# Kernel optimization log

Measured on AMD Instinct MI355X. Metric: run time of the kernel, lower is better.

The kernel has to match this reference:

```python
import jax, jax.numpy as jnp
import numpy as np
from jax import lax

B, C, H, W = 4, 1024, 25, 25
CH = [1, 10, 10, 1]  # NeighConsensus channels
K = 3                # 4D kernel size (3,3,3,3)


def setup_inputs() -> dict:
    key = jax.random.key(0)
    ks = jax.random.split(key, 8)
    inp = {
        "feature_A": jax.random.normal(ks[0], (B, C, H, W), jnp.float32),
        "feature_B": jax.random.normal(ks[1], (B, C, H, W), jnp.float32),
    }
    for i in range(3):
        cin, cout = CH[i], CH[i + 1]
        scale = 1.0 / np.sqrt(cin * K ** 4)
        inp[f"W{i+1}"] = jax.random.normal(ks[2 + 2 * i], (cout, cin, K, K, K, K), jnp.float32) * scale
        inp[f"b{i+1}"] = jnp.zeros((cout,), jnp.float32)
    return inp


def feature_l2norm(x, axis=1):
    # torch: x / sqrt(sum(x^2, dim)+1e-6)
    return x / jnp.sqrt(jnp.sum(x * x, axis=axis, keepdims=True) + 1e-6)


# 4D convolution: lhs [B,C,f1,f2,f3,f4], rhs [Cout,Cin,k,k,k,k]
_DN = lax.ConvDimensionNumbers(lhs_spec=(0, 1, 2, 3, 4, 5),
                               rhs_spec=(0, 1, 2, 3, 4, 5),
                               out_spec=(0, 1, 2, 3, 4, 5))


def conv4d(x, w, b):
    p = K // 2
    y = lax.conv_general_dilated(x, w, (1, 1, 1, 1), [(p, p)] * 4, dimension_numbers=_DN)
    return y + b[None, :, None, None, None, None]


def nc_stack(x, Ws, bs):
    # Conv4d + ReLU stack (CreateCon4D)
    for w, b in zip(Ws, bs):
        x = jax.nn.relu(conv4d(x, w, b))
    return x


def neigh_consensus(x, Ws, bs):
    # symmetric_mode: conv(x) + permuted conv of the (AB)->(BA) swapped tensor
    perm = (0, 1, 4, 5, 2, 3)
    return nc_stack(x, Ws, bs) + jnp.transpose(nc_stack(jnp.transpose(x, perm), Ws, bs), perm)


def mutual_matching(corr):
    # corr: [B,1,f1,f2,f3,f4]
    eps = 1e-5
    max_B = jnp.max(corr, axis=(2, 3), keepdims=True)  # max over (f1,f2)
    max_A = jnp.max(corr, axis=(4, 5), keepdims=True)  # max over (f3,f4)
    return corr * (corr / (max_A + eps)) * (corr / (max_B + eps))


def correlation(fA, fB):
    # FeatureCorrelation with normalization=True
    corr = jnp.einsum('bchw,bcij->bhwij', fA, fB)[:, None]  # [B,1,hA,wA,hB,wB]
    corr = jax.nn.relu(corr)
    # featureL2Norm over the singleton channel dim == elementwise x/sqrt(x^2+eps)
    return corr / jnp.sqrt(corr * corr + 1e-6)


def reference(feature_A, feature_B, W1, b1, W2, b2, W3, b3):
    fA = feature_l2norm(feature_A)
    fB = feature_l2norm(feature_B)
    corr4d = correlation(fA, fB)
    corr4d = mutual_matching(corr4d)
    corr4d = neigh_consensus(corr4d, (W1, W2, W3), (b1, b2, b3))
    corr4d = mutual_matching(corr4d)
    return corr4d
```

## Files before the change

kernel.cpp:

```cpp
#include <hip/hip_runtime.h>
#include <math.h>

#define HWQ 625
#define NPOSQ 390625
#define NB 4
#define NCH 1024

typedef __attribute__((ext_vector_type(8))) short bf16x8;
typedef __attribute__((ext_vector_type(4))) float f32x4;

__device__ inline unsigned short f2bf(float x) {
    union { float f; unsigned int u; } c; c.f = x;
    unsigned int u = c.u;
    return (unsigned short)((u + 0x7fffu + ((u >> 16) & 1u)) >> 16);
}

__global__ void pack_misc_kernel(const float* __restrict__ W1, const float* __restrict__ b1,
                                 const float* __restrict__ b2,
                                 float* __restrict__ W1P, float* __restrict__ bL1,
                                 float* __restrict__ bL2)
{
    int t = blockIdx.x * blockDim.x + threadIdx.x;
    if (t < 1620) {
        int co = t % 20; int r = t / 20; int e = r / 9, t34 = r % 9;
        W1P[t] = (co < 10) ? W1[co * 81 + e * 9 + t34] : W1[(co - 10) * 81 + t34 * 9 + e];
    }
    if (t < 20) { bL1[t] = b1[t % 10]; bL2[t] = b2[t % 10]; }
}

__global__ void pack_mfma_w2_kernel(const float* __restrict__ W2,
                                    unsigned short* __restrict__ Ablob)
{
    int t = blockIdx.x * blockDim.x + threadIdx.x;
    if (t >= 54 * 64) return;
    int frag = t >> 6, lane = t & 63;
    int g = frag / 27; int r1 = frag % 27; int kstep = r1 / 9; int dd = r1 % 9;
    int d3 = dd / 3, d4 = dd % 3;
    int co = lane & 15;
    unsigned short v[8];
#pragma unroll
    for (int j = 0; j < 8; ++j) {
        int k = kstep * 32 + ((lane >> 4) << 3) + j;
        float w = 0.0f;
        if (co < 10 && k < 90) {
            int ci = k / 9, e = k % 9, d1 = e / 3, d2 = e % 3;
            int tap = (g == 0) ? (d1 * 27 + d2 * 9 + d3 * 3 + d4)
                               : (d3 * 27 + d4 * 9 + d1 * 3 + d2);
            w = W2[(co * 10 + ci) * 81 + tap];
        }
        v[j] = f2bf(w);
    }
    uint4 val;
    val.x = (unsigned)v[0] | ((unsigned)v[1] << 16);
    val.y = (unsigned)v[2] | ((unsigned)v[3] << 16);
    val.z = (unsigned)v[4] | ((unsigned)v[5] << 16);
    val.w = (unsigned)v[6] | ((unsigned)v[7] << 16);
    *(uint4*)(Ablob + (size_t)frag * 512 + lane * 8) = val;
}

__global__ void pack_mfma_w3_kernel(const float* __restrict__ W3,
                                    unsigned short* __restrict__ Ablob3)
{
    int t = blockIdx.x * blockDim.x + threadIdx.x;
    if (t >= 54 * 64) return;
    int frag = t >> 6, lane = t & 63;
    int kstep = frag / 9, dd = frag % 9;
    int d3 = dd / 3, d4 = dd % 3;
    int row = lane & 15;
    unsigned short v[8];
#pragma unroll
    for (int j = 0; j < 8; ++j) {
        int k = kstep * 32 + ((lane >> 4) << 3) + j;
        float w = 0.0f;
        if (k < 180) {
            int g = k / 90, rem = k - g * 90;
            int ci = rem / 9, e = rem % 9;
            if (row == g) {
                int d1 = e / 3, d2 = e % 3;
                int tap = (g == 0) ? (d1 * 27 + d2 * 9 + d3 * 3 + d4)
                                   : (d3 * 27 + d4 * 9 + d1 * 3 + d2);
                w = W3[ci * 81 + tap];
            }
        }
        v[j] = f2bf(w);
    }
    uint4 val;
    val.x = (unsigned)v[0] | ((unsigned)v[1] << 16);
    val.y = (unsigned)v[2] | ((unsigned)v[3] << 16);
    val.z = (unsigned)v[4] | ((unsigned)v[5] << 16);
    val.w = (unsigned)v[6] | ((unsigned)v[7] << 16);
    *(uint4*)(Ablob3 + (size_t)frag * 512 + lane * 8) = val;
}

__global__ void invnorm_kernel(const float* __restrict__ fA, const float* __restrict__ fB,
                               float* __restrict__ invA, float* __restrict__ invB)
{
    int idx = blockIdx.x * blockDim.x + threadIdx.x;
    if (idx >= NB * HWQ) return;
    const float* f = blockIdx.y ? fB : fA;
    float* o = blockIdx.y ? invB : invA;
    int b = idx / HWQ, m = idx - b * HWQ;
    const float* p = f + (size_t)b * NCH * HWQ + m;
    float s = 0.f;
    for (int c = 0; c < NCH; c += 4) {
        float x0 = p[(c + 0) * HWQ], x1 = p[(c + 1) * HWQ];
        float x2 = p[(c + 2) * HWQ], x3 = p[(c + 3) * HWQ];
        s += x0 * x0 + x1 * x1 + x2 * x2 + x3 * x3;
    }
    o[idx] = 1.0f / sqrtf(s + 1e-6f);
}

__global__ __launch_bounds__(256) void corr_gemm_kernel(
    const float* __restrict__ fA, const float* __restrict__ fB,
    const float* __restrict__ invA, const float* __restrict__ invB,
    float* __restrict__ corr)
{
    __shared__ float As[16][64];
    __shared__ float Bs[16][64];
    const int b = blockIdx.z;
    const int m0 = blockIdx.y * 64, n0 = blockIdx.x * 64;
    const int tid = threadIdx.x;
    const int tx = tid & 15, ty = tid >> 4;
    float acc[4][4] = {};
    const float* Ab = fA + (size_t)b * NCH * HWQ;
    const float* Bb = fB + (size_t)b * NCH * HWQ;
    for (int k0 = 0; k0 < NCH; k0 += 16) {
        for (int i = tid; i < 1024; i += 256) {
            int k = i >> 6, mm = i & 63;
            int gm = m0 + mm, gn = n0 + mm;
            As[k][mm] = (gm < HWQ) ? Ab[(k0 + k) * HWQ + gm] : 0.0f;
            Bs[k][mm] = (gn < HWQ) ? Bb[(k0 + k) * HWQ + gn] : 0.0f;
        }
        __syncthreads();
#pragma unroll
        for (int k = 0; k < 16; ++k) {
            float4 a4 = *(const float4*)&As[k][ty * 4];
            float4 b4 = *(const float4*)&Bs[k][tx * 4];
            float av[4] = {a4.x, a4.y, a4.z, a4.w};
            float bv[4] = {b4.x, b4.y, b4.z, b4.w};
#pragma unroll
            for (int i = 0; i < 4; ++i)
#pragma unroll
                for (int j = 0; j < 4; ++j)
                    acc[i][j] = fmaf(av[i], bv[j], acc[i][j]);
        }
        __syncthreads();
    }
#pragma unroll
    for (int i = 0; i < 4; ++i) {
        int m = m0 + ty * 4 + i;
        if (m >= HWQ) continue;
        float ia = invA[b * HWQ + m];
#pragma unroll
        for (int j = 0; j < 4; ++j) {
            int n = n0 + tx * 4 + j;
            if (n >= HWQ) continue;
            float v = acc[i][j] * ia * invB[b * HWQ + n];
            v = fmaxf(v, 0.0f);
            v = v / sqrtf(v * v + 1e-6f);
            corr[((size_t)b * HWQ + m) * HWQ + n] = v;
        }
    }
}

__global__ void rowmax_kernel(const float* __restrict__ s, float* __restrict__ rmax)
{
    int row = blockIdx.x * 4 + (threadIdx.x >> 6);
    int lane = threadIdx.x & 63;
    if (row >= NB * HWQ) return;
    const float* p = s + (size_t)row * HWQ;
    float v = -1e30f;
    for (int n = lane; n < HWQ; n += 64) v = fmaxf(v, p[n]);
    for (int off = 32; off; off >>= 1) v = fmaxf(v, __shfl_xor(v, off));
    if (lane == 0) rmax[row] = v;
// ... 31 lines not shown
    const float* in = corr + (size_t)blockIdx.z * NPOSQ;
    unsigned short* out = x1 + (size_t)blockIdx.z * 20 * NPOSQ;
    const int f1 = f12 / 25, f2 = f12 - f1 * 25;
    const int tid = threadIdx.x;

    for (int i = tid; i < 9 * 784; i += 192) sp[i] = 0.0f;
    for (int i = tid; i < 1620; i += 192) wl[i] = W1P[i];

    const int tt = (tid < 169) ? tid : 0;
    const int ty = tt / 13, tx = tt - ty * 13;
    const int r0 = ty * 2, c0 = tx * 2;

    float acc[20][4];
#pragma unroll
    for (int co = 0; co < 20; ++co) {
        float bv = bL1[co];
        acc[co][0] = bv; acc[co][1] = bv; acc[co][2] = bv; acc[co][3] = bv;
    }

    __syncthreads();
    for (int i = tid; i < 5625; i += 192) {
        int e = i / 625, q = i - e * 625;
        int d1 = e / 3, d2 = e - d1 * 3;
        int f1n = f1 + d1 - 1, f2n = f2 + d2 - 1;
        float v = 0.0f;
        if (((unsigned)f1n < 25u) & ((unsigned)f2n < 25u))
            v = in[(f1n * 25 + f2n) * HWQ + q];
        int rr = q / 25, cc = q - rr * 25;
        sp[e * 784 + (rr + 1) * 28 + (cc + 1)] = v;
    }
    __syncthreads();

#pragma unroll 1
    for (int e = 0; e < 9; ++e) {
        float win[16];
        const int base = e * 784 + r0 * 28 + c0;
#pragma unroll
        for (int a = 0; a < 4; ++a)
#pragma unroll
            for (int bb = 0; bb < 4; ++bb)
                win[a * 4 + bb] = sp[base + a * 28 + bb];
#pragma unroll
        for (int t34 = 0; t34 < 9; ++t34) {
            int d3 = t34 / 3, d4 = t34 - d3 * 3;
            float x0 = win[d3 * 4 + d4], x1v = win[d3 * 4 + d4 + 1];
            float x2v = win[(d3 + 1) * 4 + d4], x3v = win[(d3 + 1) * 4 + d4 + 1];
            const float* wp = wl + (e * 9 + t34) * 20;
#pragma unroll
            for (int c4 = 0; c4 < 5; ++c4) {
                float4 w4 = *(const float4*)(wp + c4 * 4);
                float wv[4] = {w4.x, w4.y, w4.z, w4.w};
#pragma unroll
                for (int q4 = 0; q4 < 4; ++q4) {
                    int co = c4 * 4 + q4;
                    acc[co][0] = fmaf(x0, wv[q4], acc[co][0]);
                    acc[co][1] = fmaf(x1v, wv[q4], acc[co][1]);
                    acc[co][2] = fmaf(x2v, wv[q4], acc[co][2]);
                    acc[co][3] = fmaf(x3v, wv[q4], acc[co][3]);
                }
            }
        }
    }

    if (tid < 169) {
        unsigned short* ob = out + (size_t)f12 * 20 * 625;
#pragma unroll
        for (int co = 0; co < 20; ++co) {
            unsigned short* op = ob + co * 625;
#pragma unroll
            for (int i = 0; i < 2; ++i)
#pragma unroll
                for (int j = 0; j < 2; ++j) {
                    int f3 = r0 + i, f4 = c0 + j;
                    if (f3 < 25 && f4 < 25)
                        op[f3 * 25 + f4] = f2bf(fmaxf(acc[co][i * 2 + j], 0.0f));
                }
        }
    }
}

#define L2S 36
#define L2ROWS 736

#define STAGE_PRE()                                                         \
    int dstw_[10];                                                          \
    _Pragma("unroll")                                                       \
    for (int pass = 0; pass < 10; ++pass) {                                 \
        int idx = pass * 64 + lane;                                         \
        int rr = idx / 25, cc = idx - rr * 25;                              \
        dstw_[pass] = ((rr + 1) * 27 + cc + 1) * (L2S * 2) + wave * 8;      \
    }                                                                       \
    unsigned bpo_[7];                                                       \
    _Pragma("unroll")                                                       \
    for (int j = 0; j < 7; ++j) {                                           \
        int t = wave + j * 8;                                               \
        int f3 = t >> 1, h = t & 1;                                         \
        bpo_[j] = (unsigned)(((f3 * 27 + h * 16 + lo16) * L2S + kqg) * 2);  \
    }

#define STAGE_KSTEP(INPTR, CHOFF, CIE_MAX)                                  \
    _Pragma("unroll")                                                       \
    for (int i = 0; i < 4; ++i) {                                           \
        int cie = ksbase + wave * 4 + i;                                    \
        int ci = cie / 9, e = cie - ci * 9;                                 \
        int f1n = f1 + e / 3 - 1, f2n = f2 + (e - (e / 3) * 3) - 1;         \
        bool valid = (cie < (CIE_MAX)) & ((unsigned)f1n < 25u) & ((unsigned)f2n < 25u); \
        int pidx = valid ? ((f1n * 25 + f2n) * 20 + (CHOFF) + ci) : 0;      \
        const unsigned short* gp = (INPTR) + (size_t)pidx * 625;            \
        _Pragma("unroll")                                                   \
        for (int pass = 0; pass < 10; ++pass) {                             \
            if (pass < 9 || lane < 49) {                                    \
                unsigned short v = valid ? gp[pass * 64 + lane] : (unsigned short)0; \
                *(unsigned short*)((char*)sp + (dstw_[pass] + i * 2)) = v;  \
            }                                                               \
        }                                                                   \
    }

#define MFMA_KSTEP(ABASE)                                                   \
    {                                                                       \
        bf16x8 afA = *(const bf16x8*)(ABASE);                               \
        _Pragma("unroll")                                                   \
        for (int dd = 0; dd < 9; ++dd) {                                    \
            bf16x8 afN = (dd < 8) ? *(const bf16x8*)((ABASE) + (dd + 1) * 512) : afA; \
            const int d3 = dd / 3, d4 = dd - d3 * 3;                        \
            const int imm = (d3 * 27 + d4) * (L2S * 2);                     \
            _Pragma("unroll")                                               \
            for (int j = 0; j < 7; ++j) {                                   \
                if (j < 6 || wave < 2) {                                    \
                    const char* rp = (const char*)sp + (bpo_[j] + imm);     \
                    uint2 p0 = *(const uint2*)rp;                           \
                    uint2 p1 = *(const uint2*)(rp + 8);                     \
                    union { unsigned u[4]; bf16x8 v; } cv;                  \
                    cv.u[0] = p0.x; cv.u[1] = p0.y; cv.u[2] = p1.x; cv.u[3] = p1.y; \
                    acc[j] = __builtin_amdgcn_mfma_f32_16x16x32_bf16(afA, cv.v, acc[j], 0, 0, 0); \
                }                                                           \
            }                                                               \
            afA = afN;                                                      \
        }                                                                   \
    }

__global__ __launch_bounds__(512) void conv4d_mfma_l2(
    const unsigned short* __restrict__ x1, const unsigned short* __restrict__ Ablob,
    const float* __restrict__ bL2, unsigned short* __restrict__ x2)
{
    __shared__ alignas(16) unsigned short sp[L2ROWS * L2S];
    const int f12 = blockIdx.x, g = blockIdx.y;
    const unsigned short* in = x1 + (size_t)blockIdx.z * 20 * NPOSQ;
    unsigned short* out = x2 + (size_t)blockIdx.z * 20 * NPOSQ;
    const int f1 = f12 / 25, f2 = f12 - f1 * 25;
    const int tid = threadIdx.x, wave = tid >> 6, lane = tid & 63;
    const int lo16 = lane & 15, kqg = (lane >> 4) << 3;

    for (int i = tid; i < L2ROWS * L2S / 2; i += 512) ((unsigned*)sp)[i] = 0u;

    f32x4 acc[7];
#pragma unroll
    for (int j = 0; j < 7; ++j) acc[j] = (f32x4){0.f, 0.f, 0.f, 0.f};
    const unsigned short* Ag = Ablob + (size_t)g * 27 * 512;

    STAGE_PRE();

#pragma unroll 1
    for (int kstep = 0; kstep < 3; ++kstep) {
        const int ksbase = kstep * 32;
        __syncthreads();
        STAGE_KSTEP(in, g * 10, 90);
        __syncthreads();
        const unsigned short* Abase = Ag + (size_t)(kstep * 9) * 512 + lane * 8;
        MFMA_KSTEP(Abase);
    }

    unsigned short* ob = out + (size_t)f12 * 20 * 625 + g * 10 * 625;
    int t = wave;
    for (int j = 0; j < 7; ++j, t += 8) {
        if (t < 50) {
            int f3 = t >> 1, h = t & 1;
            int f4 = h * 16 + lo16;
            if (f4 < 25) {
#pragma unroll
                for (int r = 0; r < 4; ++r) {
                    int co = (lane >> 4) * 4 + r;
                    if (co < 10) {
                        float v = acc[j][r] + bL2[g * 10 + co];
                        ob[co * 625 + f3 * 25 + f4] = f2bf(fmaxf(v, 0.0f));
                    }
                }
            }
        }
    }
}

__global__ __launch_bounds__(512) void conv4d_mfma_l3(
    const unsigned short* __restrict__ x2, const unsigned short* __restrict__ Ablob3,
    const float* __restrict__ b3p, float* __restrict__ sbuf)
{
    __shared__ alignas(16) unsigned short sp[L2ROWS * L2S];
    const int f12 = blockIdx.x;
    const unsigned short* in = x2 + (size_t)blockIdx.z * 20 * NPOSQ;
    float* out = sbuf + (size_t)blockIdx.z * NPOSQ;
    const int f1 = f12 / 25, f2 = f12 - f1 * 25;
    const int tid = threadIdx.x, wave = tid >> 6, lane = tid & 63;
    const int lo16 = lane & 15, kqg = (lane >> 4) << 3;

    for (int i = tid; i < L2ROWS * L2S / 2; i += 512) ((unsigned*)sp)[i] = 0u;

    f32x4 acc[7];
#pragma unroll
    for (int j = 0; j < 7; ++j) acc[j] = (f32x4){0.f, 0.f, 0.f, 0.f};

    STAGE_PRE();

#pragma unroll 1
    for (int kstep = 0; kstep < 6; ++kstep) {
        const int ksbase = kstep * 32;
        __syncthreads();
        STAGE_KSTEP(in, 0, 180);
        __syncthreads();
        const unsigned short* Abase = Ablob3 + (size_t)(kstep * 9) * 512 + lane * 8;
        MFMA_KSTEP(Abase);
    }

    const float b3v = b3p[0];
    if ((lane >> 4) == 0) {
        int t = wave;
        for (int j = 0; j < 7; ++j, t += 8) {
            if (t < 50) {
                int f3 = t >> 1, h = t & 1;
                int f4 = h * 16 + lo16;
                if (f4 < 25) {
                    float s0 = fmaxf(acc[j][0] + b3v, 0.0f);
                    float s1 = fmaxf(acc[j][1] + b3v, 0.0f);
                    out[f12 * 625 + f3 * 25 + f4] = s0 + s1;
                }
            }
        }
    }
}

extern "C" void kernel_launch(void* const* d_in, const int* in_sizes, int n_in,
                              void* d_out, int out_size, void* d_ws, size_t ws_size,
                              hipStream_t stream)
{
    const float* fA = (const float*)d_in[0];
    const float* fB = (const float*)d_in[1];
    const float* W1 = (const float*)d_in[2];
    const float* b1 = (const float*)d_in[3];
    const float* W2 = (const float*)d_in[4];
    const float* b2 = (const float*)d_in[5];
    const float* W3 = (const float*)d_in[6];
    const float* b3 = (const float*)d_in[7];
    float* out = (float*)d_out;
    float* ws = (float*)d_ws;

    float* invA = ws + 0;
    float* invB = ws + 2500;
    float* rmax = ws + 5000;
    float* cmax = ws + 7500;
    float* W1P  = ws + 10000;
    float* bL1  = ws + 11620;
    float* bL2  = ws + 11640;
    unsigned short* Ablob2 = (unsigned short*)(ws + 12000);
    unsigned short* Ablob3 = (unsigned short*)(ws + 25824);
    float* corr = ws + 40000;
    float* sbuf = ws + 1602500;
    unsigned short* x1b = (unsigned short*)(ws + 3165000);

    const size_t REQ = (size_t)34415000 * 4;
    const bool fused = ws_size >= REQ;
    unsigned short* x2b = fused ? (unsigned short*)(ws + 18790000)
                                : (unsigned short*)(ws + 7080000);

    hipLaunchKernelGGL(pack_misc_kernel, dim3(7), dim3(256), 0, stream, W1, b1, b2, W1P, bL1, bL2);
    hipLaunchKernelGGL(pack_mfma_w2_kernel, dim3(14), dim3(256), 0, stream, W2, Ablob2);
    hipLaunchKernelGGL(pack_mfma_w3_kernel, dim3(14), dim3(256), 0, stream, W3, Ablob3);
    hipLaunchKernelGGL(invnorm_kernel, dim3(10, 2), dim3(256), 0, stream, fA, fB, invA, invB);
    hipLaunchKernelGGL(corr_gemm_kernel, dim3(10, 10, 4), dim3(256), 0, stream,
                       fA, fB, invA, invB, corr);
    hipLaunchKernelGGL(rowmax_kernel, dim3(625), dim3(256), 0, stream, corr, rmax);
    hipLaunchKernelGGL(colmax_kernel, dim3(4, 5), dim3(128), 0, stream, corr, cmax);
    hipLaunchKernelGGL(mm_apply_kernel, dim3(6104), dim3(256), 0, stream, corr, rmax, cmax, corr);

    if (fused) {
        hipLaunchKernelGGL(conv4d_l1, dim3(625, 1, NB), dim3(192), 0, stream, corr, W1P, bL1, x1b);
        hipLaunchKernelGGL(conv4d_mfma_l2, dim3(625, 2, NB), dim3(512), 0, stream,
                           x1b, Ablob2, bL2, x2b);
        hipLaunchKernelGGL(conv4d_mfma_l3, dim3(625, 1, NB), dim3(512), 0, stream,
                           x2b, Ablob3, b3, sbuf);
    } else {
        for (int b = 0; b < NB; ++b) {
            hipLaunchKernelGGL(conv4d_l1, dim3(625, 1, 1), dim3(192), 0, stream,
                               corr + (size_t)b * NPOSQ, W1P, bL1, x1b);
            hipLaunchKernelGGL(conv4d_mfma_l2, dim3(625, 2, 1), dim3(512), 0, stream,
                               x1b, Ablob2, bL2, x2b);
            hipLaunchKernelGGL(conv4d_mfma_l3, dim3(625, 1, 1), dim3(512), 0, stream,
                               x2b, Ablob3, b3, sbuf + (size_t)b * NPOSQ);
        }
    }

    hipLaunchKernelGGL(rowmax_kernel, dim3(625), dim3(256), 0, stream, sbuf, rmax);
    hipLaunchKernelGGL(colmax_kernel, dim3(4, 5), dim3(128), 0, stream, sbuf, cmax);
    hipLaunchKernelGGL(mm_apply_kernel, dim3(6104), dim3(256), 0, stream, sbuf, rmax, cmax, out);
}
```

Measured before the change: 1.265 ms.

## Prefetch L2 conv inputs into registers and replace L3 MFMA with VALU conv

```diff
diff --git a/kernel.cpp b/kernel.cpp
--- a/kernel.cpp
+++ b/kernel.cpp
@@ -14,16 +14,22 @@
     unsigned int u = c.u;
     return (unsigned short)((u + 0x7fffu + ((u >> 16) & 1u)) >> 16);
 }
+__device__ inline float bfl(unsigned u) { union { unsigned v; float f; } c; c.v = u << 16; return c.f; }
+__device__ inline float bfh(unsigned u) { union { unsigned v; float f; } c; c.v = u & 0xffff0000u; return c.f; }
 
 __global__ void pack_misc_kernel(const float* __restrict__ W1, const float* __restrict__ b1,
-                                 const float* __restrict__ b2,
-                                 float* __restrict__ W1P, float* __restrict__ bL1,
-                                 float* __restrict__ bL2)
+                                 const float* __restrict__ b2, const float* __restrict__ W3,
+                                 float* __restrict__ W1P, float* __restrict__ W3V,
+                                 float* __restrict__ bL1, float* __restrict__ bL2)
 {
     int t = blockIdx.x * blockDim.x + threadIdx.x;
     if (t < 1620) {
         int co = t % 20; int r = t / 20; int e = r / 9, t34 = r % 9;
         W1P[t] = (co < 10) ? W1[co * 81 + e * 9 + t34] : W1[(co - 10) * 81 + t34 * 9 + e];
+    }
+    if (t < 1620) {
+        int g = t / 810; int rem = t - g * 810; int ci = rem / 81; int tap = rem - ci * 81;
+        W3V[t] = W3[ci * 81 + (g == 0 ? tap : (tap % 9) * 9 + tap / 9)];
     }
     if (t < 20) { bL1[t] = b1[t % 10]; bL2[t] = b2[t % 10]; }
 }
@@ -56,40 +62,6 @@
     val.z = (unsigned)v[4] | ((unsigned)v[5] << 16);
     val.w = (unsigned)v[6] | ((unsigned)v[7] << 16);
     *(uint4*)(Ablob + (size_t)frag * 512 + lane * 8) = val;
-}
-
-__global__ void pack_mfma_w3_kernel(const float* __restrict__ W3,
-                                    unsigned short* __restrict__ Ablob3)
-{
-    int t = blockIdx.x * blockDim.x + threadIdx.x;
-    if (t >= 54 * 64) return;
-    int frag = t >> 6, lane = t & 63;
-    int kstep = frag / 9, dd = frag % 9;
-    int d3 = dd / 3, d4 = dd % 3;
-    int row = lane & 15;
-    unsigned short v[8];
-#pragma unroll
-    for (int j = 0; j < 8; ++j) {
-        int k = kstep * 32 + ((lane >> 4) << 3) + j;
-        float w = 0.0f;
-        if (k < 180) {
-            int g = k / 90, rem = k - g * 90;
-            int ci = rem / 9, e = rem % 9;
-            if (row == g) {
-                int d1 = e / 3, d2 = e % 3;
-                int tap = (g == 0) ? (d1 * 27 + d2 * 9 + d3 * 3 + d4)
-                                   : (d3 * 27 + d4 * 9 + d1 * 3 + d2);
-                w = W3[ci * 81 + tap];
-            }
-        }
-        v[j] = f2bf(w);
-    }
-    uint4 val;
-    val.x = (unsigned)v[0] | ((unsigned)v[1] << 16);
-    val.y = (unsigned)v[2] | ((unsigned)v[3] << 16);
-    val.z = (unsigned)v[4] | ((unsigned)v[5] << 16);
-    val.w = (unsigned)v[6] | ((unsigned)v[7] << 16);
-    *(uint4*)(Ablob3 + (size_t)frag * 512 + lane * 8) = val;
 }
 
 __global__ void invnorm_kernel(const float* __restrict__ fA, const float* __restrict__ fB,
@@ -287,60 +259,30 @@
 #define L2S 36
 #define L2ROWS 736
 
-#define STAGE_PRE()                                                         \
-    int dstw_[10];                                                          \
+#define L2_CALC(KS)                                                         \
+    {                                                                       \
+        int ksb = (KS) * 32;                                                \
+        _Pragma("unroll")                                                   \
+        for (int i2 = 0; i2 < 4; ++i2) {                                    \
+            int cie = ksb + wave * 4 + i2;                                  \
+            int ci = cie / 9, e = cie - ci * 9;                             \
+            int f1n = f1 + e / 3 - 1, f2n = f2 + (e - (e / 3) * 3) - 1;     \
+            bool valid = (cie < 90) & ((unsigned)f1n < 25u) & ((unsigned)f2n < 25u); \
+            int pidx = valid ? ((f1n * 25 + f2n) * 20 + g * 10 + ci) : 0;   \
+            gpp[i2] = in + (size_t)pidx * 625;                              \
+            vld[i2] = valid;                                                \
+        }                                                                   \
+    }
+
+#define L2_LOAD()                                                           \
     _Pragma("unroll")                                                       \
     for (int pass = 0; pass < 10; ++pass) {                                 \
-        int idx = pass * 64 + lane;                                         \
-        int rr = idx / 25, cc = idx - rr * 25;                              \
-        dstw_[pass] = ((rr + 1) * 27 + cc + 1) * (L2S * 2) + wave * 8;      \
-    }                                                                       \
-    unsigned bpo_[7];                                                       \
-    _Pragma("unroll")                                                       \
-    for (int j = 0; j < 7; ++j) {                                           \
-        int t = wave + j * 8;                                               \
-        int f3 = t >> 1, h = t & 1;                                         \
-        bpo_[j] = (unsigned)(((f3 * 27 + h * 16 + lo16) * L2S + kqg) * 2);  \
-    }
-
-#define STAGE_KSTEP(INPTR, CHOFF, CIE_MAX)                                  \
-    _Pragma("unroll")                                                       \
-    for (int i = 0; i < 4; ++i) {                                           \
-        int cie = ksbase + wave * 4 + i;                                    \
-        int ci = cie / 9, e = cie - ci * 9;                                 \
-        int f1n = f1 + e / 3 - 1, f2n = f2 + (e - (e / 3) * 3) - 1;         \
-        bool valid = (cie < (CIE_MAX)) & ((unsigned)f1n < 25u) & ((unsigned)f2n < 25u); \
-        int pidx = valid ? ((f1n * 25 + f2n) * 20 + (CHOFF) + ci) : 0;      \
-        const unsigned short* gp = (INPTR) + (size_t)pidx * 625;            \
-        _Pragma("unroll")                                                   \
-        for (int pass = 0; pass < 10; ++pass) {                             \
-            if (pass < 9 || lane < 49) {                                    \
-                unsigned short v = valid ? gp[pass * 64 + lane] : (unsigned short)0; \
-                *(unsigned short*)((char*)sp + (dstw_[pass] + i * 2)) = v;  \
-            }                                                               \
-        }                                                                   \
-    }
-
-#define MFMA_KSTEP(ABASE)                                                   \
-    {                                                                       \
-        bf16x8 afA = *(const bf16x8*)(ABASE);                               \
-        _Pragma("unroll")                                                   \
-        for (int dd = 0; dd < 9; ++dd) {                                    \
-            bf16x8 afN = (dd < 8) ? *(const bf16x8*)((ABASE) + (dd + 1) * 512) : afA; \
-            const int d3 = dd / 3, d4 = dd - d3 * 3;                        \
-            const int imm = (d3 * 27 + d4) * (L2S * 2);                     \
-            _Pragma("unroll")                                               \
-            for (int j = 0; j < 7; ++j) {                                   \
-                if (j < 6 || wave < 2) {                                    \
-                    const char* rp = (const char*)sp + (bpo_[j] + imm);     \
-                    uint2 p0 = *(const uint2*)rp;                           \
-                    uint2 p1 = *(const uint2*)(rp + 8);                     \
-                    union { unsigned u[4]; bf16x8 v; } cv;                  \
-                    cv.u[0] = p0.x; cv.u[1] = p0.y; cv.u[2] = p1.x; cv.u[3] = p1.y; \
-                    acc[j] = __builtin_amdgcn_mfma_f32_16x16x32_bf16(afA, cv.v, acc[j], 0, 0, 0); \
-                }                                                           \
-            }                                                               \
-            afA = afN;                                                      \
+        if (pass < 9 || lane < 49) {                                        \
+            int q = pass * 64 + lane;                                       \
+            vreg[pass][0] = vld[0] ? gpp[0][q] : (unsigned short)0;         \
+            vreg[pass][1] = vld[1] ? gpp[1][q] : (unsigned short)0;         \
+            vreg[pass][2] = vld[2] ? gpp[2][q] : (unsigned short)0;         \
+            vreg[pass][3] = vld[3] ? gpp[3][q] : (unsigned short)0;         \
         }                                                                   \
     }
 
@@ -363,16 +305,66 @@
     for (int j = 0; j < 7; ++j) acc[j] = (f32x4){0.f, 0.f, 0.f, 0.f};
     const unsigned short* Ag = Ablob + (size_t)g * 27 * 512;
 
-    STAGE_PRE();
+    int dstw_[10];
+#pragma unroll
+    for (int pass = 0; pass < 10; ++pass) {
+        int idx = pass * 64 + lane;
+        int rr = idx / 25, cc = idx - rr * 25;
+        dstw_[pass] = ((rr + 1) * 27 + cc + 1) * (L2S * 2) + wave * 8;
+    }
+    unsigned bpo_[7];
+#pragma unroll
+    for (int j = 0; j < 7; ++j) {
+        int t = wave + j * 8;
+        int f3 = t >> 1, h = t & 1;
+        bpo_[j] = (unsigned)(((f3 * 27 + h * 16 + lo16) * L2S + kqg) * 2);
+    }
+
+    const unsigned short* gpp[4];
+    bool vld[4];
+    unsigned short vreg[10][4];
+
+    L2_CALC(0);
+    L2_LOAD();
 
 #pragma unroll 1
     for (int kstep = 0; kstep < 3; ++kstep) {
-        const int ksbase = kstep * 32;
         __syncthreads();
-        STAGE_KSTEP(in, g * 10, 90);
+#pragma unroll
+        for (int pass = 0; pass < 10; ++pass) {
+            if (pass < 9 || lane < 49) {
+                uint2 w;
+                w.x = (unsigned)vreg[pass][0] | ((unsigned)vreg[pass][1] << 16);
+                w.y = (unsigned)vreg[pass][2] | ((unsigned)vreg[pass][3] << 16);
+                *(uint2*)((char*)sp + dstw_[pass]) = w;
+            }
+        }
         __syncthreads();
         const unsigned short* Abase = Ag + (size_t)(kstep * 9) * 512 + lane * 8;
-        MFMA_KSTEP(Abase);
+        bf16x8 af[9];
+#pragma unroll
+        for (int dd = 0; dd < 9; ++dd)
+            af[dd] = *(const bf16x8*)(Abase + dd * 512);
+        if (kstep < 2) {
+            L2_CALC(kstep + 1);
+            L2_LOAD();
+        }
+#pragma unroll
+        for (int dd = 0; dd < 9; ++dd) {
+            const int d3 = dd / 3, d4 = dd - d3 * 3;
+            const int imm = (d3 * 27 + d4) * (L2S * 2);
+#pragma unroll
+            for (int j = 0; j < 7; ++j) {
+                if (j < 6 || wave < 2) {
+                    const char* rp = (const char*)sp + (bpo_[j] + imm);
+                    uint2 p0 = *(const uint2*)rp;
+                    uint2 p1 = *(const uint2*)(rp + 8);
+                    union { unsigned u[4]; bf16x8 v; } cv;
+                    cv.u[0] = p0.x; cv.u[1] = p0.y; cv.u[2] = p1.x; cv.u[3] = p1.y;
+                    acc[j] = __builtin_amdgcn_mfma_f32_16x16x32_bf16(af[dd], cv.v, acc[j], 0, 0, 0);
+                }
+            }
+        }
     }
 
     unsigned short* ob = out + (size_t)f12 * 20 * 625 + g * 10 * 625;
@@ -395,50 +387,89 @@
     }
 }
 
-__global__ __launch_bounds__(512) void conv4d_mfma_l3(
-    const unsigned short* __restrict__ x2, const unsigned short* __restrict__ Ablob3,
+__global__ __launch_bounds__(192) void conv4d_l3_valu(
+    const unsigned short* __restrict__ x2, const float* __restrict__ W3V,
     const float* __restrict__ b3p, float* __restrict__ sbuf)
 {
-    __shared__ alignas(16) unsigned short sp[L2ROWS * L2S];
+    __shared__ unsigned short spb[2 * 9 * 784];
+    __shared__ float wl[1620];
     const int f12 = blockIdx.x;
     const unsigned short* in = x2 + (size_t)blockIdx.z * 20 * NPOSQ;
     float* out = sbuf + (size_t)blockIdx.z * NPOSQ;
     const int f1 = f12 / 25, f2 = f12 - f1 * 25;
-    const int tid = threadIdx.x, wave = tid >> 6, lane = tid & 63;
-    const int lo16 = lane & 15, kqg = (lane >> 4) << 3;
-
-    for (int i = tid; i < L2ROWS * L2S / 2; i += 512) ((unsigned*)sp)[i] = 0u;
-
-    f32x4 acc[7];
-#pragma unroll
-    for (int j = 0; j < 7; ++j) acc[j] = (f32x4){0.f, 0.f, 0.f, 0.f};
-
-    STAGE_PRE();
+    const int tid = threadIdx.x;
+
+    for (int i = tid; i < 2 * 9 * 784; i += 192) spb[i] = 0;
+    for (int i = tid; i < 1620; i += 192) wl[i] = W3V[i];
+
+    const int tt = (tid < 169) ? tid : 0;
+    const int ty = tt / 13, tx = tt - ty * 13;
+    const int r0 = ty * 2, c0 = tx * 2;
+
+    float acc0[4] = {0.f, 0.f, 0.f, 0.f}, acc1[4] = {0.f, 0.f, 0.f, 0.f};
 
 #pragma unroll 1
-    for (int kstep = 0; kstep < 6; ++kstep) {
-        const int ksbase = kstep * 32;
+    for (int ci = 0; ci < 10; ++ci) {
         __syncthreads();
-        STAGE_KSTEP(in, 0, 180);
+        for (int i = tid; i < 11250; i += 192) {
+            int plane = i / 625, q = i - plane * 625;
+            int gg = plane / 9, e = plane - gg * 9;
+            int d1 = e / 3, d2 = e - d1 * 3;
+            int f1n = f1 + d1 - 1, f2n = f2 + d2 - 1;
+            unsigned short v = 0;
+            if (((unsigned)f1n < 25u) & ((unsigned)f2n < 25u))
+                v = in[((size_t)(f1n * 25 + f2n) * 20 + gg * 10 + ci) * 625 + q];
+            int rr = q / 25, cc = q - rr * 25;
+            spb[plane * 784 + (rr + 1) * 28 + cc + 1] = v;
+        }
         __syncthreads();
-        const unsigned short* Abase = Ablob3 + (size_t)(kstep * 9) * 512 + lane * 8;
-        MFMA_KSTEP(Abase);
+        const float* w0p = wl + ci * 81;
+        const float* w1p = wl + (10 + ci) * 81;
+#pragma unroll 1
+        for (int e = 0; e < 9; ++e) {
+            float wa[16], wb[16];
+            const int base = e * 784 + r0 * 28 + c0;
+            const unsigned* pA = (const unsigned*)(spb + base);
+            const unsigned* pB = (const unsigned*)(spb + 9 * 784 + base);
+#pragma unroll
+            for (int a = 0; a < 4; ++a) {
+                unsigned uA0 = pA[a * 14], uA1 = pA[a * 14 + 1];
+                unsigned uB0 = pB[a * 14], uB1 = pB[a * 14 + 1];
+                wa[a * 4 + 0] = bfl(uA0); wa[a * 4 + 1] = bfh(uA0);
+                wa[a * 4 + 2] = bfl(uA1); wa[a * 4 + 3] = bfh(uA1);
+                wb[a * 4 + 0] = bfl(uB0); wb[a * 4 + 1] = bfh(uB0);
+                wb[a * 4 + 2] = bfl(uB1); wb[a * 4 + 3] = bfh(uB1);
+            }
+#pragma unroll
+            for (int t34 = 0; t34 < 9; ++t34) {
+                int d3 = t34 / 3, d4 = t34 - d3 * 3;
+                float g0w = w0p[e * 9 + t34];
+                float g1w = w1p[e * 9 + t34];
+                acc0[0] = fmaf(wa[d3 * 4 + d4],           g0w, acc0[0]);
+                acc0[1] = fmaf(wa[d3 * 4 + d4 + 1],       g0w, acc0[1]);
+                acc0[2] = fmaf(wa[(d3 + 1) * 4 + d4],     g0w, acc0[2]);
+                acc0[3] = fmaf(wa[(d3 + 1) * 4 + d4 + 1], g0w, acc0[3]);
+                acc1[0] = fmaf(wb[d3 * 4 + d4],           g1w, acc1[0]);
+                acc1[1] = fmaf(wb[d3 * 4 + d4 + 1],       g1w, acc1[1]);
+                acc1[2] = fmaf(wb[(d3 + 1) * 4 + d4],     g1w, acc1[2]);
+                acc1[3] = fmaf(wb[(d3 + 1) * 4 + d4 + 1], g1w, acc1[3]);
+            }
+        }
     }
 
     const float b3v = b3p[0];
-    if ((lane >> 4) == 0) {
-        int t = wave;
-        for (int j = 0; j < 7; ++j, t += 8) {
-            if (t < 50) {
-                int f3 = t >> 1, h = t & 1;
-                int f4 = h * 16 + lo16;
-                if (f4 < 25) {
-                    float s0 = fmaxf(acc[j][0] + b3v, 0.0f);
-                    float s1 = fmaxf(acc[j][1] + b3v, 0.0f);
-                    out[f12 * 625 + f3 * 25 + f4] = s0 + s1;
+    if (tid < 169) {
+#pragma unroll
+        for (int i = 0; i < 2; ++i)
+#pragma unroll
+            for (int j = 0; j < 2; ++j) {
+                int f3 = r0 + i, f4 = c0 + j;
+                if (f3 < 25 && f4 < 25) {
+                    int qi = i * 2 + j;
+                    out[f12 * 625 + f3 * 25 + f4] =
+                        fmaxf(acc0[qi] + b3v, 0.0f) + fmaxf(acc1[qi] + b3v, 0.0f);
                 }
             }
-        }
     }
 }
 
@@ -465,7 +496,7 @@
     float* bL1  = ws + 11620;
     float* bL2  = ws + 11640;
     unsigned short* Ablob2 = (unsigned short*)(ws + 12000);
-    unsigned short* Ablob3 = (unsigned short*)(ws + 25824);
+    float* W3V  = ws + 25824;
     float* corr = ws + 40000;
     float* sbuf = ws + 1602500;
     unsigned short* x1b = (unsigned short*)(ws + 3165000);
@@ -475,9 +506,9 @@
     unsigned short* x2b = fused ? (unsigned short*)(ws + 18790000)
                                 : (unsigned short*)(ws + 7080000);
 
-    hipLaunchKernelGGL(pack_misc_kernel, dim3(7), dim3(256), 0, stream, W1, b1, b2, W1P, bL1, bL2);
+    hipLaunchKernelGGL(pack_misc_kernel, dim3(7), dim3(256), 0, stream,
+                       W1, b1, b2, W3, W1P, W3V, bL1, bL2);
     hipLaunchKernelGGL(pack_mfma_w2_kernel, dim3(14), dim3(256), 0, stream, W2, Ablob2);
-    hipLaunchKernelGGL(pack_mfma_w3_kernel, dim3(14), dim3(256), 0, stream, W3, Ablob3);
     hipLaunchKernelGGL(invnorm_kernel, dim3(10, 2), dim3(256), 0, stream, fA, fB, invA, invB);
     hipLaunchKernelGGL(corr_gemm_kernel, dim3(10, 10, 4), dim3(256), 0, stream,
                        fA, fB, invA, invB, corr);
@@ -489,16 +520,16 @@
         hipLaunchKernelGGL(conv4d_l1, dim3(625, 1, NB), dim3(192), 0, stream, corr, W1P, bL1, x1b);
         hipLaunchKernelGGL(conv4d_mfma_l2, dim3(625, 2, NB), dim3(512), 0, stream,
                            x1b, Ablob2, bL2, x2b);
-        hipLaunchKernelGGL(conv4d_mfma_l3, dim3(625, 1, NB), dim3(512), 0, stream,
-                           x2b, Ablob3, b3, sbuf);
+        hipLaunchKernelGGL(conv4d_l3_valu, dim3(625, 1, NB), dim3(192), 0, stream,
+                           x2b, W3V, b3, sbuf);
     } else {
         for (int b = 0; b < NB; ++b) {
             hipLaunchKernelGGL(conv4d_l1, dim3(625, 1, 1), dim3(192), 0, stream,
                                corr + (size_t)b * NPOSQ, W1P, bL1, x1b);
             hipLaunchKernelGGL(conv4d_mfma_l2, dim3(625, 2, 1), dim3(512), 0, stream,
                                x1b, Ablob2, bL2, x2b);
-            hipLaunchKernelGGL(conv4d_mfma_l3, dim3(625, 1, 1), dim3(512), 0, stream,
-                               x2b, Ablob3, b3, sbuf + (size_t)b * NPOSQ);
+            hipLaunchKernelGGL(conv4d_l3_valu, dim3(625, 1, 1), dim3(192), 0, stream,
+                               x2b, W3V, b3, sbuf + (size_t)b * NPOSQ);
         }
     }
 
```

After: 1.586 ms. 1.25x slower.

## Prefetch next k-step global loads into registers while running MFMAs

Applied to the files above, without the earlier changes.

```diff
diff --git a/kernel.cpp b/kernel.cpp
--- a/kernel.cpp
+++ b/kernel.cpp
@@ -287,7 +287,7 @@
 #define L2S 36
 #define L2ROWS 736
 
-#define STAGE_PRE()                                                         \
+#define MF_PRE()                                                            \
     int dstw_[10];                                                          \
     _Pragma("unroll")                                                       \
     for (int pass = 0; pass < 10; ++pass) {                                 \
@@ -301,46 +301,64 @@
         int t = wave + j * 8;                                               \
         int f3 = t >> 1, h = t & 1;                                         \
         bpo_[j] = (unsigned)(((f3 * 27 + h * 16 + lo16) * L2S + kqg) * 2);  \
-    }
-
-#define STAGE_KSTEP(INPTR, CHOFF, CIE_MAX)                                  \
+    }                                                                       \
+    const unsigned short* gpp[4];                                           \
+    bool vld[4];                                                            \
+    unsigned short vreg[10][4];
+
+#define MF_CALC(KS, CHOFF, CIE_MAX)                                         \
+    {                                                                       \
+        int ksb = (KS) * 32;                                                \
+        _Pragma("unroll")                                                   \
+        for (int i2 = 0; i2 < 4; ++i2) {                                    \
+            int cie = ksb + wave * 4 + i2;                                  \
+            int e = cie % 9;                                                \
+            int f1n = f1 + e / 3 - 1, f2n = f2 + (e - (e / 3) * 3) - 1;     \
+            bool valid = (cie < (CIE_MAX)) & ((unsigned)f1n < 25u) & ((unsigned)f2n < 25u); \
+            int pidx = valid ? ((f1n * 25 + f2n) * 20 + (CHOFF) + cie / 9) : 0; \
+            gpp[i2] = in + (size_t)pidx * 625;                              \
+            vld[i2] = valid;                                                \
+        }                                                                   \
+    }
+
+#define MF_LOAD()                                                           \
     _Pragma("unroll")                                                       \
-    for (int i = 0; i < 4; ++i) {                                           \
-        int cie = ksbase + wave * 4 + i;                                    \
-        int ci = cie / 9, e = cie - ci * 9;                                 \
-        int f1n = f1 + e / 3 - 1, f2n = f2 + (e - (e / 3) * 3) - 1;         \
-        bool valid = (cie < (CIE_MAX)) & ((unsigned)f1n < 25u) & ((unsigned)f2n < 25u); \
-        int pidx = valid ? ((f1n * 25 + f2n) * 20 + (CHOFF) + ci) : 0;      \
-        const unsigned short* gp = (INPTR) + (size_t)pidx * 625;            \
+    for (int pass = 0; pass < 10; ++pass) {                                 \
+        if (pass < 9 || lane < 49) {                                        \
+            int q = pass * 64 + lane;                                       \
+            vreg[pass][0] = vld[0] ? gpp[0][q] : (unsigned short)0;         \
+            vreg[pass][1] = vld[1] ? gpp[1][q] : (unsigned short)0;         \
+            vreg[pass][2] = vld[2] ? gpp[2][q] : (unsigned short)0;         \
+            vreg[pass][3] = vld[3] ? gpp[3][q] : (unsigned short)0;         \
+        }                                                                   \
+    }
+
+#define MF_WRITE()                                                          \
+    _Pragma("unroll")                                                       \
+    for (int pass = 0; pass < 10; ++pass) {                                 \
+        if (pass < 9 || lane < 49) {                                        \
+            uint2 w;                                                        \
+            w.x = (unsigned)vreg[pass][0] | ((unsigned)vreg[pass][1] << 16);\
+            w.y = (unsigned)vreg[pass][2] | ((unsigned)vreg[pass][3] << 16);\
+            *(uint2*)((char*)sp + dstw_[pass]) = w;                         \
+        }                                                                   \
+    }
+
+#define MF_MFMA(AF)                                                         \
+    _Pragma("unroll")                                                       \
+    for (int dd = 0; dd < 9; ++dd) {                                        \
+        const int d3 = dd / 3, d4 = dd - d3 * 3;                            \
+        const int imm = (d3 * 27 + d4) * (L2S * 2);                         \
         _Pragma("unroll")                                                   \
-        for (int pass = 0; pass < 10; ++pass) {                             \
-            if (pass < 9 || lane < 49) {                                    \
-                unsigned short v = valid ? gp[pass * 64 + lane] : (unsigned short)0; \
-                *(unsigned short*)((char*)sp + (dstw_[pass] + i * 2)) = v;  \
+        for (int j = 0; j < 7; ++j) {                                       \
+            if (j < 6 || wave < 2) {                                        \
+                const char* rp = (const char*)sp + (bpo_[j] + imm);         \
+                uint2 p0 = *(const uint2*)rp;                               \
+                uint2 p1 = *(const uint2*)(rp + 8);                         \
+                union { unsigned u[4]; bf16x8 v; } cv;                      \
+                cv.u[0] = p0.x; cv.u[1] = p0.y; cv.u[2] = p1.x; cv.u[3] = p1.y; \
+                acc[j] = __builtin_amdgcn_mfma_f32_16x16x32_bf16((AF)[dd], cv.v, acc[j], 0, 0, 0); \
             }                                                               \
-        }                                                                   \
-    }
-
-#define MFMA_KSTEP(ABASE)                                                   \
-    {                                                                       \
-        bf16x8 afA = *(const bf16x8*)(ABASE);                               \
-        _Pragma("unroll")                                                   \
-        for (int dd = 0; dd < 9; ++dd) {                                    \
-            bf16x8 afN = (dd < 8) ? *(const bf16x8*)((ABASE) + (dd + 1) * 512) : afA; \
-            const int d3 = dd / 3, d4 = dd - d3 * 3;                        \
-            const int imm = (d3 * 27 + d4) * (L2S * 2);                     \
-            _Pragma("unroll")                                               \
-            for (int j = 0; j < 7; ++j) {                                   \
-                if (j < 6 || wave < 2) {                                    \
-                    const char* rp = (const char*)sp + (bpo_[j] + imm);     \
-                    uint2 p0 = *(const uint2*)rp;                           \
-                    uint2 p1 = *(const uint2*)(rp + 8);                     \
-                    union { unsigned u[4]; bf16x8 v; } cv;                  \
-                    cv.u[0] = p0.x; cv.u[1] = p0.y; cv.u[2] = p1.x; cv.u[3] = p1.y; \
-                    acc[j] = __builtin_amdgcn_mfma_f32_16x16x32_bf16(afA, cv.v, acc[j], 0, 0, 0); \
-                }                                                           \
-            }                                                               \
-            afA = afN;                                                      \
         }                                                                   \
     }
 
@@ -363,16 +381,25 @@
     for (int j = 0; j < 7; ++j) acc[j] = (f32x4){0.f, 0.f, 0.f, 0.f};
     const unsigned short* Ag = Ablob + (size_t)g * 27 * 512;
 
-    STAGE_PRE();
+    MF_PRE();
+    MF_CALC(0, g * 10, 90);
+    MF_LOAD();
 
 #pragma unroll 1
     for (int kstep = 0; kstep < 3; ++kstep) {
-        const int ksbase = kstep * 32;
         __syncthreads();
-        STAGE_KSTEP(in, g * 10, 90);
+        MF_WRITE();
         __syncthreads();
         const unsigned short* Abase = Ag + (size_t)(kstep * 9) * 512 + lane * 8;
-        MFMA_KSTEP(Abase);
+        bf16x8 af[9];
+#pragma unroll
+        for (int dd = 0; dd < 9; ++dd)
+            af[dd] = *(const bf16x8*)(Abase + dd * 512);
+        if (kstep < 2) {
+            MF_CALC(kstep + 1, g * 10, 90);
+            MF_LOAD();
+        }
+        MF_MFMA(af);
     }
 
     unsigned short* ob = out + (size_t)f12 * 20 * 625 + g * 10 * 625;
@@ -413,16 +440,25 @@
 #pragma unroll
     for (int j = 0; j < 7; ++j) acc[j] = (f32x4){0.f, 0.f, 0.f, 0.f};
 
-    STAGE_PRE();
+    MF_PRE();
+    MF_CALC(0, 0, 180);
+    MF_LOAD();
 
 #pragma unroll 1
     for (int kstep = 0; kstep < 6; ++kstep) {
-        const int ksbase = kstep * 32;
         __syncthreads();
-        STAGE_KSTEP(in, 0, 180);
+        MF_WRITE();
         __syncthreads();
         const unsigned short* Abase = Ablob3 + (size_t)(kstep * 9) * 512 + lane * 8;
-        MFMA_KSTEP(Abase);
+        bf16x8 af[9];
+#pragma unroll
+        for (int dd = 0; dd < 9; ++dd)
+            af[dd] = *(const bf16x8*)(Abase + dd * 512);
+        if (kstep < 5) {
+            MF_CALC(kstep + 1, 0, 180);
+            MF_LOAD();
+        }
+        MF_MFMA(af);
     }
 
     const float b3v = b3p[0];
@@ -475,7 +511,8 @@
     unsigned short* x2b = fused ? (unsigned short*)(ws + 18790000)
                                 : (unsigned short*)(ws + 7080000);
 
-    hipLaunchKernelGGL(pack_misc_kernel, dim3(7), dim3(256), 0, stream, W1, b1, b2, W1P, bL1, bL2);
+    hipLaunchKernelGGL(pack_misc_kernel, dim3(7), dim3(256), 0, stream,
+                       W1, b1, b2, W1P, bL1, bL2);
     hipLaunchKernelGGL(pack_mfma_w2_kernel, dim3(14), dim3(256), 0, stream, W2, Ablob2);
     hipLaunchKernelGGL(pack_mfma_w3_kernel, dim3(14), dim3(256), 0, stream, W3, Ablob3);
     hipLaunchKernelGGL(invnorm_kernel, dim3(10, 2), dim3(256), 0, stream, fA, fB, invA, invB);
```

Measured after the change: 1.110 ms. 1.14x faster.

## Restructure layer-3 conv as 32x32 MFMA over taps with shared-memory shift-sum epilogue

Applied to the files above, without the earlier changes.

```diff
diff --git a/kernel.cpp b/kernel.cpp
--- a/kernel.cpp
+++ b/kernel.cpp
@@ -8,6 +8,7 @@
 
 typedef __attribute__((ext_vector_type(8))) short bf16x8;
 typedef __attribute__((ext_vector_type(4))) float f32x4;
+typedef __attribute__((ext_vector_type(16))) float f32x16;
 
 __device__ inline unsigned short f2bf(float x) {
     union { float f; unsigned int u; } c; c.f = x;
@@ -62,21 +63,21 @@
                                     unsigned short* __restrict__ Ablob3)
 {
     int t = blockIdx.x * blockDim.x + threadIdx.x;
-    if (t >= 54 * 64) return;
+    if (t >= 12 * 64) return;
     int frag = t >> 6, lane = t & 63;
-    int kstep = frag / 9, dd = frag % 9;
-    int d3 = dd / 3, d4 = dd % 3;
-    int row = lane & 15;
+    int chunk = frag >> 1, s = frag & 1;
+    int m = lane & 31;
     unsigned short v[8];
 #pragma unroll
     for (int j = 0; j < 8; ++j) {
-        int k = kstep * 32 + ((lane >> 4) << 3) + j;
+        int k = chunk * 32 + s * 16 + ((lane >> 5) << 3) + j;
         float w = 0.0f;
-        if (k < 180) {
-            int g = k / 90, rem = k - g * 90;
-            int ci = rem / 9, e = rem % 9;
-            if (row == g) {
-                int d1 = e / 3, d2 = e % 3;
+        if (m < 18 && k < 180) {
+            int g = m / 9, dd = m % 9;
+            int ch = k / 9, e = k % 9;
+            if (ch / 10 == g) {
+                int ci = ch % 10;
+                int d1 = e / 3, d2 = e % 3, d3 = dd / 3, d4 = dd % 3;
                 int tap = (g == 0) ? (d1 * 27 + d2 * 9 + d3 * 3 + d4)
                                    : (d3 * 27 + d4 * 9 + d1 * 3 + d2);
                 w = W3[ci * 81 + tap];
@@ -287,63 +288,6 @@
 #define L2S 36
 #define L2ROWS 736
 
-#define STAGE_PRE()                                                         \
-    int dstw_[10];                                                          \
-    _Pragma("unroll")                                                       \
-    for (int pass = 0; pass < 10; ++pass) {                                 \
-        int idx = pass * 64 + lane;                                         \
-        int rr = idx / 25, cc = idx - rr * 25;                              \
-        dstw_[pass] = ((rr + 1) * 27 + cc + 1) * (L2S * 2) + wave * 8;      \
-    }                                                                       \
-    unsigned bpo_[7];                                                       \
-    _Pragma("unroll")                                                       \
-    for (int j = 0; j < 7; ++j) {                                           \
-        int t = wave + j * 8;                                               \
-        int f3 = t >> 1, h = t & 1;                                         \
-        bpo_[j] = (unsigned)(((f3 * 27 + h * 16 + lo16) * L2S + kqg) * 2);  \
-    }
-
-#define STAGE_KSTEP(INPTR, CHOFF, CIE_MAX)                                  \
-    _Pragma("unroll")                                                       \
-    for (int i = 0; i < 4; ++i) {                                           \
-        int cie = ksbase + wave * 4 + i;                                    \
-        int ci = cie / 9, e = cie - ci * 9;                                 \
-        int f1n = f1 + e / 3 - 1, f2n = f2 + (e - (e / 3) * 3) - 1;         \
-        bool valid = (cie < (CIE_MAX)) & ((unsigned)f1n < 25u) & ((unsigned)f2n < 25u); \
-        int pidx = valid ? ((f1n * 25 + f2n) * 20 + (CHOFF) + ci) : 0;      \
-        const unsigned short* gp = (INPTR) + (size_t)pidx * 625;            \
-        _Pragma("unroll")                                                   \
-        for (int pass = 0; pass < 10; ++pass) {                             \
-            if (pass < 9 || lane < 49) {                                    \
-                unsigned short v = valid ? gp[pass * 64 + lane] : (unsigned short)0; \
-                *(unsigned short*)((char*)sp + (dstw_[pass] + i * 2)) = v;  \
-            }                                                               \
-        }                                                                   \
-    }
-
-#define MFMA_KSTEP(ABASE)                                                   \
-    {                                                                       \
-        bf16x8 afA = *(const bf16x8*)(ABASE);                               \
-        _Pragma("unroll")                                                   \
-        for (int dd = 0; dd < 9; ++dd) {                                    \
-            bf16x8 afN = (dd < 8) ? *(const bf16x8*)((ABASE) + (dd + 1) * 512) : afA; \
-            const int d3 = dd / 3, d4 = dd - d3 * 3;                        \
-            const int imm = (d3 * 27 + d4) * (L2S * 2);                     \
-            _Pragma("unroll")                                               \
-            for (int j = 0; j < 7; ++j) {                                   \
-                if (j < 6 || wave < 2) {                                    \
-                    const char* rp = (const char*)sp + (bpo_[j] + imm);     \
-                    uint2 p0 = *(const uint2*)rp;                           \
-                    uint2 p1 = *(const uint2*)(rp + 8);                     \
-                    union { unsigned u[4]; bf16x8 v; } cv;                  \
-                    cv.u[0] = p0.x; cv.u[1] = p0.y; cv.u[2] = p1.x; cv.u[3] = p1.y; \
-                    acc[j] = __builtin_amdgcn_mfma_f32_16x16x32_bf16(afA, cv.v, acc[j], 0, 0, 0); \
-                }                                                           \
-            }                                                               \
-            afA = afN;                                                      \
-        }                                                                   \
-    }
-
 __global__ __launch_bounds__(512) void conv4d_mfma_l2(
     const unsigned short* __restrict__ x1, const unsigned short* __restrict__ Ablob,
     const float* __restrict__ bL2, unsigned short* __restrict__ x2)
@@ -363,16 +307,74 @@
     for (int j = 0; j < 7; ++j) acc[j] = (f32x4){0.f, 0.f, 0.f, 0.f};
     const unsigned short* Ag = Ablob + (size_t)g * 27 * 512;
 
-    STAGE_PRE();
+    int dstw_[10];
+#pragma unroll
+    for (int pass = 0; pass < 10; ++pass) {
+        int idx = pass * 64 + lane;
+        int rr = idx / 25, cc = idx - rr * 25;
+        dstw_[pass] = ((rr + 1) * 27 + cc + 1) * (L2S * 2) + wave * 8;
+    }
+    unsigned bpo_[7];
+#pragma unroll
+    for (int j = 0; j < 7; ++j) {
+        int t = wave + j * 8;
+        int f3 = t >> 1, h = t & 1;
+        bpo_[j] = (unsigned)(((f3 * 27 + h * 16 + lo16) * L2S + kqg) * 2);
+    }
 
 #pragma unroll 1
     for (int kstep = 0; kstep < 3; ++kstep) {
-        const int ksbase = kstep * 32;
+        const unsigned short* gpp[4];
+        bool vld[4];
+        {
+            int ksb = kstep * 32;
+#pragma unroll
+            for (int i2 = 0; i2 < 4; ++i2) {
+                int cie = ksb + wave * 4 + i2;
+                int e = cie % 9;
+                int f1n = f1 + e / 3 - 1, f2n = f2 + (e % 3) - 1;
+                bool valid = (cie < 90) & ((unsigned)f1n < 25u) & ((unsigned)f2n < 25u);
+                int pidx = valid ? ((f1n * 25 + f2n) * 20 + g * 10 + cie / 9) : 0;
+                gpp[i2] = in + (size_t)pidx * 625;
+                vld[i2] = valid;
+            }
+        }
         __syncthreads();
-        STAGE_KSTEP(in, g * 10, 90);
+#pragma unroll
+        for (int pass = 0; pass < 10; ++pass) {
+            if (pass < 9 || lane < 49) {
+                int q = pass * 64 + lane;
+                unsigned short v0 = vld[0] ? gpp[0][q] : (unsigned short)0;
+                unsigned short v1 = vld[1] ? gpp[1][q] : (unsigned short)0;
+                unsigned short v2 = vld[2] ? gpp[2][q] : (unsigned short)0;
+                unsigned short v3 = vld[3] ? gpp[3][q] : (unsigned short)0;
+                uint2 w;
+                w.x = (unsigned)v0 | ((unsigned)v1 << 16);
+                w.y = (unsigned)v2 | ((unsigned)v3 << 16);
+                *(uint2*)((char*)sp + dstw_[pass]) = w;
+            }
+        }
         __syncthreads();
         const unsigned short* Abase = Ag + (size_t)(kstep * 9) * 512 + lane * 8;
-        MFMA_KSTEP(Abase);
+        bf16x8 afA = *(const bf16x8*)(Abase);
+#pragma unroll
+        for (int dd = 0; dd < 9; ++dd) {
+            bf16x8 afN = (dd < 8) ? *(const bf16x8*)(Abase + (dd + 1) * 512) : afA;
+            const int d3 = dd / 3, d4 = dd - d3 * 3;
+            const int imm = (d3 * 27 + d4) * (L2S * 2);
+#pragma unroll
+            for (int j = 0; j < 7; ++j) {
+                if (j < 6 || wave < 2) {
+                    const char* rp = (const char*)sp + (bpo_[j] + imm);
+                    uint2 p0 = *(const uint2*)rp;
+                    uint2 p1 = *(const uint2*)(rp + 8);
+                    union { unsigned u[4]; bf16x8 v; } cv;
+                    cv.u[0] = p0.x; cv.u[1] = p0.y; cv.u[2] = p1.x; cv.u[3] = p1.y;
+                    acc[j] = __builtin_amdgcn_mfma_f32_16x16x32_bf16(afA, cv.v, acc[j], 0, 0, 0);
+                }
+            }
+            afA = afN;
+        }
     }
 
     unsigned short* ob = out + (size_t)f12 * 20 * 625 + g * 10 * 625;
@@ -405,40 +407,102 @@
     float* out = sbuf + (size_t)blockIdx.z * NPOSQ;
     const int f1 = f12 / 25, f2 = f12 - f1 * 25;
     const int tid = threadIdx.x, wave = tid >> 6, lane = tid & 63;
-    const int lo16 = lane & 15, kqg = (lane >> 4) << 3;
+    const int col = lane & 31, kg8 = (lane >> 5) << 3;
 
     for (int i = tid; i < L2ROWS * L2S / 2; i += 512) ((unsigned*)sp)[i] = 0u;
 
-    f32x4 acc[7];
-#pragma unroll
-    for (int j = 0; j < 7; ++j) acc[j] = (f32x4){0.f, 0.f, 0.f, 0.f};
-
-    STAGE_PRE();
+    f32x16 acc0 = {}, acc1 = {}, acc2 = {};
+    const int t0 = wave, t1 = wave + 8, t2 = wave + 16;
+    const bool has2 = (t2 < 23);
+
+    int dstw_[10];
+#pragma unroll
+    for (int pass = 0; pass < 10; ++pass) {
+        int idx = pass * 64 + lane;
+        int rr = idx / 25, cc = idx - rr * 25;
+        dstw_[pass] = ((rr + 1) * 27 + cc + 1) * (L2S * 2) + wave * 8;
+    }
+    const unsigned short* b0p = sp + (t0 * 32 + col) * L2S + kg8;
+    const unsigned short* b1p = sp + (t1 * 32 + col) * L2S + kg8;
+    const unsigned short* b2p = sp + (t2 * 32 + col) * L2S + kg8;
 
 #pragma unroll 1
-    for (int kstep = 0; kstep < 6; ++kstep) {
-        const int ksbase = kstep * 32;
+    for (int chunk = 0; chunk < 6; ++chunk) {
+        const unsigned short* gpp[4];
+        bool vld[4];
+        {
+            int ksb = chunk * 32;
+#pragma unroll
+            for (int i2 = 0; i2 < 4; ++i2) {
+                int cie = ksb + wave * 4 + i2;
+                int e = cie % 9;
+                int f1n = f1 + e / 3 - 1, f2n = f2 + (e % 3) - 1;
+                bool valid = (cie < 180) & ((unsigned)f1n < 25u) & ((unsigned)f2n < 25u);
+                int pidx = valid ? ((f1n * 25 + f2n) * 20 + cie / 9) : 0;
+                gpp[i2] = in + (size_t)pidx * 625;
+                vld[i2] = valid;
+            }
+        }
         __syncthreads();
-        STAGE_KSTEP(in, 0, 180);
+#pragma unroll
+        for (int pass = 0; pass < 10; ++pass) {
+            if (pass < 9 || lane < 49) {
+                int q = pass * 64 + lane;
+                unsigned short v0 = vld[0] ? gpp[0][q] : (unsigned short)0;
+                unsigned short v1 = vld[1] ? gpp[1][q] : (unsigned short)0;
+                unsigned short v2 = vld[2] ? gpp[2][q] : (unsigned short)0;
+                unsigned short v3 = vld[3] ? gpp[3][q] : (unsigned short)0;
+                uint2 w;
+                w.x = (unsigned)v0 | ((unsigned)v1 << 16);
+                w.y = (unsigned)v2 | ((unsigned)v3 << 16);
+                *(uint2*)((char*)sp + dstw_[pass]) = w;
+            }
+        }
         __syncthreads();
-        const unsigned short* Abase = Ablob3 + (size_t)(kstep * 9) * 512 + lane * 8;
-        MFMA_KSTEP(Abase);
-    }
+        bf16x8 a0 = *(const bf16x8*)(Ablob3 + (size_t)(chunk * 2 + 0) * 512 + lane * 8);
+        bf16x8 a1 = *(const bf16x8*)(Ablob3 + (size_t)(chunk * 2 + 1) * 512 + lane * 8);
+        bf16x8 b;
+        b = *(const bf16x8*)(b0p);
+        acc0 = __builtin_amdgcn_mfma_f32_32x32x16_bf16(a0, b, acc0, 0, 0, 0);
+        b = *(const bf16x8*)(b0p + 16);
+        acc0 = __builtin_amdgcn_mfma_f32_32x32x16_bf16(a1, b, acc0, 0, 0, 0);
+        b = *(const bf16x8*)(b1p);
+        acc1 = __builtin_amdgcn_mfma_f32_32x32x16_bf16(a0, b, acc1, 0, 0, 0);
+        b = *(const bf16x8*)(b1p + 16);
+        acc1 = __builtin_amdgcn_mfma_f32_32x32x16_bf16(a1, b, acc1, 0, 0, 0);
+        if (has2) {
+            b = *(const bf16x8*)(b2p);
+            acc2 = __builtin_amdgcn_mfma_f32_32x32x16_bf16(a0, b, acc2, 0, 0, 0);
+            b = *(const bf16x8*)(b2p + 16);
+            acc2 = __builtin_amdgcn_mfma_f32_32x32x16_bf16(a1, b, acc2, 0, 0, 0);
+        }
+    }
+
+    __syncthreads();
+    float* D = (float*)sp;
+#pragma unroll
+    for (int r = 0; r < 16; ++r) {
+        int m = (r & 3) + 8 * (r >> 2) + 4 * (lane >> 5);
+        if (m < 18) {
+            D[m * L2ROWS + t0 * 32 + col] = acc0[r];
+            D[m * L2ROWS + t1 * 32 + col] = acc1[r];
+            if (has2) D[m * L2ROWS + t2 * 32 + col] = acc2[r];
+        }
+    }
+    __syncthreads();
 
     const float b3v = b3p[0];
-    if ((lane >> 4) == 0) {
-        int t = wave;
-        for (int j = 0; j < 7; ++j, t += 8) {
-            if (t < 50) {
-                int f3 = t >> 1, h = t & 1;
-                int f4 = h * 16 + lo16;
-                if (f4 < 25) {
-                    float s0 = fmaxf(acc[j][0] + b3v, 0.0f);
-                    float s1 = fmaxf(acc[j][1] + b3v, 0.0f);
-                    out[f12 * 625 + f3 * 25 + f4] = s0 + s1;
-                }
-            }
-        }
+    for (int q = tid; q < 625; q += 512) {
+        int f3 = q / 25, f4 = q - f3 * 25;
+        float s0 = 0.f, s1 = 0.f;
+#pragma unroll
+        for (int dd = 0; dd < 9; ++dd) {
+            int d3 = dd / 3, d4 = dd - d3 * 3;
+            int hq = (f3 + d3) * 27 + (f4 + d4);
+            s0 += D[dd * L2ROWS + hq];
+            s1 += D[(9 + dd) * L2ROWS + hq];
+        }
+        out[f12 * 625 + q] = fmaxf(s0 + b3v, 0.0f) + fmaxf(s1 + b3v, 0.0f);
     }
 }
 
@@ -475,9 +539,10 @@
     unsigned short* x2b = fused ? (unsigned short*)(ws + 18790000)
                                 : (unsigned short*)(ws + 7080000);
 
-    hipLaunchKernelGGL(pack_misc_kernel, dim3(7), dim3(256), 0, stream, W1, b1, b2, W1P, bL1, bL2);
+    hipLaunchKernelGGL(pack_misc_kernel, dim3(7), dim3(256), 0, stream,
+                       W1, b1, b2, W1P, bL1, bL2);
     hipLaunchKernelGGL(pack_mfma_w2_kernel, dim3(14), dim3(256), 0, stream, W2, Ablob2);
-    hipLaunchKernelGGL(pack_mfma_w3_kernel, dim3(14), dim3(256), 0, stream, W3, Ablob3);
+    hipLaunchKernelGGL(pack_mfma_w3_kernel, dim3(3), dim3(256), 0, stream, W3, Ablob3);
     hipLaunchKernelGGL(invnorm_kernel, dim3(10, 2), dim3(256), 0, stream, fA, fB, invA, invB);
     hipLaunchKernelGGL(corr_gemm_kernel, dim3(10, 10, 4), dim3(256), 0, stream,
                        fA, fB, invA, invB, corr);
```

Measured after the change: 1.105 ms. 12.7% less time.
